# Performance work log

Measured on AMD Instinct MI355X. Metric: run time of the kernel, lower is better.

Reference implementation:

```python
import jax, jax.numpy as jnp
import numpy as np
from jax import lax

B, CIN, VS, P, E, H = 1, 1, 64, 4, 64, 8
N = (VS // P) ** 3  # 4096 patches
OUT = CIN * P ** 3  # 64
SCALE = 1.0 / float(np.sqrt(E))
EPS = 1e-5


def setup_inputs() -> dict:
    key = jax.random.key(0)
    ks = jax.random.split(key, 8)
    sc = 0.02
    return {
        "voxel": jax.random.normal(ks[0], (B, CIN, VS, VS, VS), jnp.float32),
        "conv_w": jax.random.normal(ks[1], (E, CIN, P, P, P), jnp.float32) * sc,
        "conv_b": jnp.zeros((E,), jnp.float32),
        "ln_g": jnp.ones((E,), jnp.float32),
        "ln_b": jnp.zeros((E,), jnp.float32),
        "pos_emb": jax.random.normal(ks[2], (1, N, E), jnp.float32) * sc,
        "wqk": jax.random.normal(ks[3], (E, H * E), jnp.float32) * sc,
        "bqk": jnp.zeros((H * E,), jnp.float32),
        "wv": jax.random.normal(ks[4], (E, H * E), jnp.float32) * sc,
        "bv": jnp.zeros((H * E,), jnp.float32),
        "alpha": jnp.array(1.0, jnp.float32),
        "wout": jax.random.normal(ks[5], (H * E, OUT), jnp.float32) * sc,
        "bout": jnp.zeros((OUT,), jnp.float32),
    }


def reference(voxel, conv_w, conv_b, ln_g, ln_b, pos_emb, wqk, bqk, wv, bv, alpha, wout, bout):
    # VoxelPatchEmbedding: strided Conv3d -> flatten -> permute -> LayerNorm
    emb = lax.conv_general_dilated(
        voxel, conv_w, window_strides=(P, P, P), padding="VALID",
        dimension_numbers=("NCDHW", "OIDHW", "NCDHW"))
    emb = emb + conv_b[None, :, None, None, None]
    b = emb.shape[0]
    emb = emb.reshape(b, E, -1).transpose(0, 2, 1)  # [B, N, E]
    mu = jnp.mean(emb, axis=-1, keepdims=True)
    var = jnp.var(emb, axis=-1, keepdims=True)
    emb = (emb - mu) * lax.rsqrt(var + EPS) * ln_g + ln_b
    emb = emb + pos_emb

    # tied Q/K projection; heads to dim 1: [B, H, N, E]
    qk_proj = (emb @ wqk + bqk).reshape(b, -1, H, E).transpose(0, 2, 1, 3)
    q = qk_proj
    k = qk_proj
    v = (emb @ wv + bv).reshape(b, -1, H, E).transpose(0, 2, 1, 3)

    # L2 distance: q^2 + k^2 - 2 q.k^T  -> [B, H, N, N]
    q2 = jnp.sum(q * q, axis=-1, keepdims=True)           # [B,H,N,1]
    k2 = jnp.sum(k * k, axis=-1, keepdims=True)           # [B,H,N,1]
    dist = q2 + k2.transpose(0, 1, 3, 2) - 2.0 * jnp.einsum("bhnd,bhmd->bhnm", q, k)

    scores = alpha * jnp.exp(-dist) * SCALE
    attn_w = jax.nn.softmax(scores, axis=-1)
    attn = jnp.einsum("bhnm,bhmd->bhnd", attn_w, v)       # [B,H,N,E]
    attn = attn.transpose(0, 2, 1, 3).reshape(b, -1, H * E)
    return attn @ wout + bout                              # [B, N, CIN*P^3]
```

## Files before the change

kernel.cpp:

```cpp
#include <hip/hip_runtime.h>
#include <hip/hip_bf16.h>

#define NPAT 4096
#define EDIM 64
#define NH   8
#define HE   512
#define OUTD 64

typedef short bf16x8 __attribute__((ext_vector_type(8)));
typedef float f32x4  __attribute__((ext_vector_type(4)));

#if __has_builtin(__builtin_amdgcn_exp2f)
#define EXP2(x) __builtin_amdgcn_exp2f(x)
#else
#define EXP2(x) exp2f(x)
#endif

__device__ __forceinline__ ushort f2bf(float f) {
    uint u = __builtin_bit_cast(uint, f);
    return (ushort)((u + 0x7FFFu + ((u >> 16) & 1u)) >> 16);
}
__device__ __forceinline__ float bf2f(ushort b) {
    return __builtin_bit_cast(float, ((uint)b) << 16);
}

__global__ __launch_bounds__(64) void k_embed(
    const float* __restrict__ voxel,
    const float* __restrict__ conv_w,
    const float* __restrict__ conv_b,
    const float* __restrict__ ln_g, const float* __restrict__ ln_b,
    const float* __restrict__ pos,
    float* __restrict__ emb)
{
    const int n = blockIdx.x;
    const int d = n >> 8, hh = (n >> 4) & 15, ww = n & 15;
    const int t = threadIdx.x;
    __shared__ float vox[64];
    __shared__ float wsm[64 * 65];

    for (int i = t; i < 4096; i += 64) wsm[(i >> 6) * 65 + (i & 63)] = conv_w[i];
    const int i3 = t >> 4, j3 = (t >> 2) & 3, k3 = t & 3;
    vox[t] = voxel[(d * 4 + i3) * 4096 + (hh * 4 + j3) * 64 + (ww * 4 + k3)];
    __syncthreads();

    float acc = conv_b[t];
    #pragma unroll
    for (int m = 0; m < 64; m++) acc += vox[m] * wsm[t * 65 + m];

    float s1 = acc, s2 = acc * acc;
    #pragma unroll
    for (int off = 1; off < 64; off <<= 1) {
        s1 += __shfl_xor(s1, off);
        s2 += __shfl_xor(s2, off);
    }
    const float mu  = s1 * (1.0f / 64.0f);
    const float var = s2 * (1.0f / 64.0f) - mu * mu;
    const float y = (acc - mu) * rsqrtf(var + 1e-5f) * ln_g[t] + ln_b[t] + pos[n * 64 + t];
    emb[n * 64 + t] = y;
}

__global__ __launch_bounds__(256) void k_proj(
    const float* __restrict__ emb,
    const float* __restrict__ wqk, const float* __restrict__ bqk,
    const float* __restrict__ wv,  const float* __restrict__ bvv,
    ushort* __restrict__ qk_bf,
    ushort* __restrict__ vT_bf)
{
    const int n0 = blockIdx.x * 16;
    const int t = threadIdx.x;
    __shared__ float es[16][64];
    for (int i = t; i < 16 * 64; i += 256) es[i >> 6][i & 63] = emb[n0 * 64 + i];
    __syncthreads();

    const int he0 = t, he1 = t + 256;
    const float bq0 = bqk[he0], bq1 = bqk[he1];
    const float bv0 = bvv[he0], bv1 = bvv[he1];

    for (int rc = 0; rc < 2; rc++) {
        float aq0[8], aq1[8], av0[8], av1[8];
        #pragma unroll
        for (int r = 0; r < 8; r++) { aq0[r] = bq0; aq1[r] = bq1; av0[r] = bv0; av1[r] = bv1; }
        for (int e = 0; e < 64; e++) {
            const float wq0 = wqk[e * HE + he0], wq1 = wqk[e * HE + he1];
            const float wv0 = wv [e * HE + he0], wv1 = wv [e * HE + he1];
            #pragma unroll
            for (int r = 0; r < 8; r++) {
                const float x = es[rc * 8 + r][e];
                aq0[r] += x * wq0; aq1[r] += x * wq1;
                av0[r] += x * wv0; av1[r] += x * wv1;
            }
        }
        #pragma unroll
        for (int r = 0; r < 8; r++) {
            const int n = n0 + rc * 8 + r;
            qk_bf[((he0 >> 6) * NPAT + n) * 64 + (he0 & 63)] = f2bf(aq0[r]);
            qk_bf[((he1 >> 6) * NPAT + n) * 64 + (he1 & 63)] = f2bf(aq1[r]);
            vT_bf[((he0 >> 6) * 64 + (he0 & 63)) * NPAT + n] = f2bf(av0[r]);
            vT_bf[((he1 >> 6) * 64 + (he1 & 63)) * NPAT + n] = f2bf(av1[r]);
        }
    }
}

__global__ __launch_bounds__(256) void k_q2(
    const ushort* __restrict__ qk_bf, float* __restrict__ q2)
{
    const int i = blockIdx.x * 256 + threadIdx.x;
    const ushort* row = qk_bf + (size_t)i * 64;
    float s = 0.0f;
    #pragma unroll
    for (int c = 0; c < 8; c++) {
        bf16x8 v = *(const bf16x8*)(row + c * 8);
        #pragma unroll
        for (int j = 0; j < 8; j++) { float f = bf2f((ushort)v[j]); s += f * f; }
    }
    q2[i] = s;
}

__global__ __launch_bounds__(1024, 8) void k_attn(
    const ushort* __restrict__ qk,
    const ushort* __restrict__ vT,
    const float* __restrict__ q2,
    const float* __restrict__ alpha,
    float* __restrict__ attn)
{
    const int bid = blockIdx.x;
    const int h  = bid & 7;
    const int bx = bid >> 3;
    const int tid = threadIdx.x;
    const int w  = tid >> 6;
    const int u  = w & 3;
    const int rg = w >> 2;
    const int l  = tid & 63;
    const int lr = l & 15;
    const int lg = l >> 4;
    const float L2E = 1.4426950408889634f;
    const float ccl2e = alpha[0] * 0.125f * L2E;

    __shared__ ushort kv_lds[2][2][64 * 64];
    __shared__ ushort p_lds[4][16 * 64];
    __shared__ float  zpart[4][4][16];

    const ushort* qkh = qk + (size_t)h * NPAT * 64;
    const ushort* vTh = vT + (size_t)h * 64 * NPAT;
    const float*  q2h = q2 + h * NPAT;

    const int row0 = bx * 64 + rg * 16;

    bf16x8 aq0, aq1;
    {
        const ushort* qrow = qkh + (size_t)(row0 + lr) * 64 + 8 * lg;
        aq0 = *(const bf16x8*)(qrow);
        aq1 = *(const bf16x8*)(qrow + 32);
    }
    float nq2[4];
    #pragma unroll
    for (int r = 0; r < 4; r++) nq2[r] = q2h[row0 + 4 * lg + r];

    const int w8   = w & 7;
    const int srow = w8 * 8 + (l >> 3);
    const int sch  = (l & 7) ^ (srow & 7);
    const ushort* ksrc0 = qkh + (size_t)srow * 64 + sch * 8;
    const ushort* vsrc0 = vTh + (size_t)srow * NPAT + sch * 8;
#define STAGE(bufi, it)                                                          \
    do {                                                                         \
        const ushort* _src = (w < 8) ? (ksrc0 + (size_t)(it) * 4096)             \
                                     : (vsrc0 + (size_t)(it) * 64);              \
        ushort* _dst = &kv_lds[bufi][w >> 3][w8 * 512];                          \
        __builtin_amdgcn_global_load_lds(                                        \
            (const __attribute__((address_space(1))) unsigned int*)_src,         \
            (__attribute__((address_space(3))) unsigned int*)_dst, 16, 0, 0);    \
    } while (0)

    f32x4 acc = (f32x4){0.f, 0.f, 0.f, 0.f};
    float zacc[4] = {0.f, 0.f, 0.f, 0.f};

    const int x7 = (lr & 7);
    char* prg = (char*)&p_lds[rg][0];

    STAGE(0, 0);
    float k2c = q2h[u * 16 + lr];

    for (int it = 0; it < 64; ++it) {
        const int buf = it & 1;
        __syncthreads();
        if (it + 1 < 64) STAGE(buf ^ 1, it + 1);
        float k2n = (it + 1 < 64) ? q2h[(it + 1) * 64 + u * 16 + lr] : 0.f;

        {
            const ushort* kb = &kv_lds[buf][0][0];
            const int krow = u * 16 + lr;
            bf16x8 bk0 = *(const bf16x8*)(kb + krow * 64 + ((lg ^ x7) << 3));
            bf16x8 bk1 = *(const bf16x8*)(kb + krow * 64 + (((lg + 4) ^ x7) << 3));
            f32x4 sc = (f32x4){0.f, 0.f, 0.f, 0.f};
            sc = __builtin_amdgcn_mfma_f32_16x16x32_bf16(aq0, bk0, sc, 0, 0, 0);
            sc = __builtin_amdgcn_mfma_f32_16x16x32_bf16(aq1, bk1, sc, 0, 0, 0);
            #pragma unroll
            for (int r = 0; r < 4; r++) {
                const float d = nq2[r] + k2c - 2.0f * sc[r];
                const float p = EXP2(ccl2e * EXP2(-L2E * d));
                zacc[r] += p;
                const int prow = 4 * lg + r, pcol = 16 * u + lr;
                const int byteoff = prow * 128 + ((pcol * 2) ^ ((prow & 7) << 4));
                *(ushort*)(prg + byteoff) = f2bf(p);
            }
        }
        asm volatile("s_waitcnt lgkmcnt(0)" ::: "memory");
        __builtin_amdgcn_s_barrier();

        {
            const ushort* vb = &kv_lds[buf][1][0];
            const int vrow = u * 16 + lr;
            bf16x8 bv0 = *(const bf16x8*)(vb + vrow * 64 + ((lg ^ x7) << 3));
            bf16x8 bv1 = *(const bf16x8*)(vb + vrow * 64 + (((lg + 4) ^ x7) << 3));
            char* rb = prg + lr * 128;
            const int xx = x7 << 4;
            bf16x8 pa0 = *(const bf16x8*)(rb + ((16 * lg) ^ xx));
            bf16x8 pa1 = *(const bf16x8*)(rb + ((64 + 16 * lg) ^ xx));
            acc = __builtin_amdgcn_mfma_f32_16x16x32_bf16(pa0, bv0, acc, 0, 0, 0);
            acc = __builtin_amdgcn_mfma_f32_16x16x32_bf16(pa1, bv1, acc, 0, 0, 0);
        }
        k2c = k2n;
    }
#undef STAGE

    #pragma unroll
    for (int r = 0; r < 4; r++) {
        float z = zacc[r];
        z += __shfl_xor(z, 1); z += __shfl_xor(z, 2);
        z += __shfl_xor(z, 4); z += __shfl_xor(z, 8);
        if (lr == 0) zpart[rg][u][4 * lg + r] = z;
    }
    __syncthreads();
    #pragma unroll
    for (int r = 0; r < 4; r++) {
        const int row = 4 * lg + r;
        const float zt = zpart[rg][0][row] + zpart[rg][1][row] +
                         zpart[rg][2][row] + zpart[rg][3][row];
        attn[(size_t)(row0 + row) * HE + h * 64 + u * 16 + lr] = acc[r] / zt;
    }
}

__global__ __launch_bounds__(256) void k_out(
    const float* __restrict__ attn,
    const float* __restrict__ wout,
    const float* __restrict__ bout,
    float* __restrict__ out)
{
    const int n0 = blockIdx.x * 16;
    const int t = threadIdx.x;
    const int c = t & 63, rg = t >> 6;
    __shared__ float sa[16][512];
    for (int i = t; i < 16 * 512; i += 256) sa[i >> 9][i & 511] = attn[(size_t)n0 * 512 + i];
    __syncthreads();
    #pragma unroll
    for (int rr = 0; rr < 4; rr++) {
        const int r = rg * 4 + rr;
        float acc = bout[c];
        for (int k = 0; k < 512; k++) acc += sa[r][k] * wout[k * 64 + c];
        out[(size_t)(n0 + r) * 64 + c] = acc;
    }
}

extern "C" void kernel_launch(void* const* d_in, const int* in_sizes, int n_in,
                              void* d_out, int out_size, void* d_ws, size_t ws_size,
                              hipStream_t stream) {
    (void)in_sizes; (void)n_in; (void)out_size; (void)ws_size;
    const float* voxel  = (const float*)d_in[0];
    const float* conv_w = (const float*)d_in[1];
    const float* conv_b = (const float*)d_in[2];
    const float* ln_g   = (const float*)d_in[3];
    const float* ln_b   = (const float*)d_in[4];
    const float* pos    = (const float*)d_in[5];
    const float* wqk    = (const float*)d_in[6];
    const float* bqk    = (const float*)d_in[7];
    const float* wv     = (const float*)d_in[8];
    const float* bvv    = (const float*)d_in[9];
    const float* alpha  = (const float*)d_in[10];
    const float* wout   = (const float*)d_in[11];
    const float* bout   = (const float*)d_in[12];
    float* out = (float*)d_out;

    char* ws = (char*)d_ws;
    float*  emb   = (float*) (ws);
    ushort* qk_bf = (ushort*)(ws + (1u << 20));
    ushort* vT_bf = (ushort*)(ws + 5u * (1u << 20));
    float*  q2    = (float*) (ws + 9u * (1u << 20));
    float*  attn  = (float*) (ws + 9u * (1u << 20) + (128u << 10));

    k_embed<<<NPAT, 64, 0, stream>>>(voxel, conv_w, conv_b, ln_g, ln_b, pos, emb);
    k_proj<<<NPAT / 16, 256, 0, stream>>>(emb, wqk, bqk, wv, bvv, qk_bf, vT_bf);
    k_q2<<<(NH * NPAT) / 256, 256, 0, stream>>>(qk_bf, q2);
    k_attn<<<NPAT / 64 * NH, 1024, 0, stream>>>(qk_bf, vT_bf, q2, alpha, attn);
    k_out<<<NPAT / 16, 256, 0, stream>>>(attn, wout, bout, out);
}
```

Measured before the change: 226.1 us.

## Use bf16 MFMA for output projection and batch patches in embed kernel

The output projection now runs on bf16 MFMA instructions. The attention output is stored as bf16, and a new small kernel transposes wout into bf16 ahead of time. The embed kernel now handles 16 patches per 256-thread block, loading the weights into shared memory once per block instead of once per patch and reading voxels as float4. The aim is to cut the scalar FP32 GEMM cost, the attention-output traffic and the redundant weight loads, at the price of bf16 rounding in the final projection.

```diff
diff --git a/kernel.cpp b/kernel.cpp
--- a/kernel.cpp
+++ b/kernel.cpp
@@ -24,7 +24,7 @@
     return __builtin_bit_cast(float, ((uint)b) << 16);
 }
 
-__global__ __launch_bounds__(64) void k_embed(
+__global__ __launch_bounds__(256) void k_embed(
     const float* __restrict__ voxel,
     const float* __restrict__ conv_w,
     const float* __restrict__ conv_b,
@@ -32,31 +32,67 @@
     const float* __restrict__ pos,
     float* __restrict__ emb)
 {
-    const int n = blockIdx.x;
-    const int d = n >> 8, hh = (n >> 4) & 15, ww = n & 15;
+    const int b = blockIdx.x;
+    const int d = b >> 4, hh = b & 15;
     const int t = threadIdx.x;
-    __shared__ float vox[64];
-    __shared__ float wsm[64 * 65];
-
-    for (int i = t; i < 4096; i += 64) wsm[(i >> 6) * 65 + (i & 63)] = conv_w[i];
-    const int i3 = t >> 4, j3 = (t >> 2) & 3, k3 = t & 3;
-    vox[t] = voxel[(d * 4 + i3) * 4096 + (hh * 4 + j3) * 64 + (ww * 4 + k3)];
-    __syncthreads();
-
-    float acc = conv_b[t];
-    #pragma unroll
-    for (int m = 0; m < 64; m++) acc += vox[m] * wsm[t * 65 + m];
-
-    float s1 = acc, s2 = acc * acc;
-    #pragma unroll
-    for (int off = 1; off < 64; off <<= 1) {
+    __shared__ float wsm[64][65];
+    __shared__ float vox[16][64];
+
+    for (int i = t; i < 4096; i += 256) wsm[i >> 6][i & 63] = conv_w[i];
+    {
+        const int pair = t >> 4;
+        const int off4 = (t & 15) * 4;
+        const float4 v = *(const float4*)&voxel[(d * 4 + (pair >> 2)) * 4096 +
+                                                (hh * 4 + (pair & 3)) * 64 + off4];
+        *(float4*)&vox[pair][off4] = v;
+    }
+    __syncthreads();
+
+    const int wv = t >> 6;
+    const int l  = t & 63;
+    const int p  = wv * 4 + (l >> 4);
+    const int eb = l & 15;
+    const int n  = b * 16 + p;
+
+    float acc[4];
+    #pragma unroll
+    for (int o = 0; o < 4; o++) acc[o] = conv_b[eb + 16 * o];
+    for (int m = 0; m < 64; m++) {
+        const float v = vox[m >> 2][p * 4 + (m & 3)];
+        #pragma unroll
+        for (int o = 0; o < 4; o++) acc[o] += v * wsm[eb + 16 * o][m];
+    }
+
+    float s1 = acc[0] + acc[1] + acc[2] + acc[3];
+    float s2 = acc[0] * acc[0] + acc[1] * acc[1] + acc[2] * acc[2] + acc[3] * acc[3];
+    #pragma unroll
+    for (int off = 1; off < 16; off <<= 1) {
         s1 += __shfl_xor(s1, off);
         s2 += __shfl_xor(s2, off);
     }
     const float mu  = s1 * (1.0f / 64.0f);
     const float var = s2 * (1.0f / 64.0f) - mu * mu;
-    const float y = (acc - mu) * rsqrtf(var + 1e-5f) * ln_g[t] + ln_b[t] + pos[n * 64 + t];
-    emb[n * 64 + t] = y;
+    const float rs  = rsqrtf(var + 1e-5f);
+    #pragma unroll
+    for (int o = 0; o < 4; o++) {
+        const int e = eb + 16 * o;
+        emb[n * 64 + e] = (acc[o] - mu) * rs * ln_g[e] + ln_b[e] + pos[n * 64 + e];
+    }
+}
+
+__global__ __launch_bounds__(256) void k_wt(
+    const float* __restrict__ wout,
+    ushort* __restrict__ woutT)
+{
+    const int b = blockIdx.x;
+    const int t = threadIdx.x;
+    __shared__ float ld[64][65];
+    for (int i = t; i < 4096; i += 256) ld[i >> 6][i & 63] = wout[(b * 64 + (i >> 6)) * 64 + (i & 63)];
+    __syncthreads();
+    const int o = t >> 2, kb = (t & 3) * 16;
+    #pragma unroll
+    for (int j = 0; j < 16; j++)
+        woutT[o * 512 + b * 64 + kb + j] = f2bf(ld[kb + j][o]);
 }
 
 __global__ __launch_bounds__(256) void k_proj(
@@ -121,7 +157,7 @@
     const ushort* __restrict__ vT,
     const float* __restrict__ q2,
     const float* __restrict__ alpha,
-    float* __restrict__ attn)
+    ushort* __restrict__ attn)
 {
     const int bid = blockIdx.x;
     const int h  = bid & 7;
@@ -236,29 +272,39 @@
         const int row = 4 * lg + r;
         const float zt = zpart[rg][0][row] + zpart[rg][1][row] +
                          zpart[rg][2][row] + zpart[rg][3][row];
-        attn[(size_t)(row0 + row) * HE + h * 64 + u * 16 + lr] = acc[r] / zt;
+        attn[(size_t)(row0 + row) * HE + h * 64 + u * 16 + lr] = f2bf(acc[r] / zt);
     }
 }
 
 __global__ __launch_bounds__(256) void k_out(
-    const float* __restrict__ attn,
-    const float* __restrict__ wout,
+    const ushort* __restrict__ attn,
+    const ushort* __restrict__ woutT,
     const float* __restrict__ bout,
     float* __restrict__ out)
 {
     const int n0 = blockIdx.x * 16;
     const int t = threadIdx.x;
-    const int c = t & 63, rg = t >> 6;
-    __shared__ float sa[16][512];
-    for (int i = t; i < 16 * 512; i += 256) sa[i >> 9][i & 511] = attn[(size_t)n0 * 512 + i];
-    __syncthreads();
-    #pragma unroll
-    for (int rr = 0; rr < 4; rr++) {
-        const int r = rg * 4 + rr;
-        float acc = bout[c];
-        for (int k = 0; k < 512; k++) acc += sa[r][k] * wout[k * 64 + c];
-        out[(size_t)(n0 + r) * 64 + c] = acc;
-    }
+    const int w = t >> 6, l = t & 63, lr = l & 15, lg = l >> 4;
+    __shared__ ushort sa[16][520];
+
+    for (int c = t; c < 1024; c += 256) {
+        const int row = c >> 6, c8 = c & 63;
+        *(bf16x8*)&sa[row][c8 * 8] = *(const bf16x8*)&attn[(size_t)(n0 + row) * 512 + c8 * 8];
+    }
+    __syncthreads();
+
+    f32x4 acc = (f32x4){0.f, 0.f, 0.f, 0.f};
+    const ushort* bp = woutT + (size_t)(w * 16 + lr) * 512 + 8 * lg;
+    #pragma unroll
+    for (int kk = 0; kk < 16; kk++) {
+        bf16x8 a = *(const bf16x8*)&sa[lr][kk * 32 + 8 * lg];
+        bf16x8 bb = *(const bf16x8*)(bp + kk * 32);
+        acc = __builtin_amdgcn_mfma_f32_16x16x32_bf16(a, bb, acc, 0, 0, 0);
+    }
+    const float bo = bout[w * 16 + lr];
+    #pragma unroll
+    for (int r = 0; r < 4; r++)
+        out[(size_t)(n0 + 4 * lg + r) * 64 + w * 16 + lr] = acc[r] + bo;
 }
 
 extern "C" void kernel_launch(void* const* d_in, const int* in_sizes, int n_in,
@@ -281,15 +327,17 @@
     float* out = (float*)d_out;
 
     char* ws = (char*)d_ws;
-    float*  emb   = (float*) (ws);
-    ushort* qk_bf = (ushort*)(ws + (1u << 20));
-    ushort* vT_bf = (ushort*)(ws + 5u * (1u << 20));
-    float*  q2    = (float*) (ws + 9u * (1u << 20));
-    float*  attn  = (float*) (ws + 9u * (1u << 20) + (128u << 10));
-
-    k_embed<<<NPAT, 64, 0, stream>>>(voxel, conv_w, conv_b, ln_g, ln_b, pos, emb);
+    float*  emb     = (float*) (ws);
+    ushort* qk_bf   = (ushort*)(ws + (1u << 20));
+    ushort* vT_bf   = (ushort*)(ws + 5u * (1u << 20));
+    float*  q2      = (float*) (ws + 9u * (1u << 20));
+    ushort* attn_bf = (ushort*)(ws + 9u * (1u << 20) + (128u << 10));
+    ushort* woutT   = (ushort*)(ws + 13u * (1u << 20) + (128u << 10));
+
+    k_embed<<<256, 256, 0, stream>>>(voxel, conv_w, conv_b, ln_g, ln_b, pos, emb);
+    k_wt<<<8, 256, 0, stream>>>(wout, woutT);
     k_proj<<<NPAT / 16, 256, 0, stream>>>(emb, wqk, bqk, wv, bvv, qk_bf, vT_bf);
     k_q2<<<(NH * NPAT) / 256, 256, 0, stream>>>(qk_bf, q2);
-    k_attn<<<NPAT / 64 * NH, 1024, 0, stream>>>(qk_bf, vT_bf, q2, alpha, attn);
-    k_out<<<NPAT / 16, 256, 0, stream>>>(attn, wout, bout, out);
-}
+    k_attn<<<NPAT / 64 * NH, 1024, 0, stream>>>(qk_bf, vT_bf, q2, alpha, attn_bf);
+    k_out<<<NPAT / 16, 256, 0, stream>>>(attn_bf, woutT, bout, out);
+}
```

New measurement: 203.9 us. 1.11x faster.
